# Optimization experiments

Hardware: AMD Instinct MI355X
Metric: run time of the kernel (lower is better)

The kernel has to match this reference:

```python
import jax, jax.numpy as jnp
import numpy as np

N = 50000      # nodes
E = 1600000    # edges (avg degree 32)
IN, H, OUT, ED = 16, 128, 64, 16


def setup_inputs() -> dict:
    key = jax.random.key(0)
    ks = jax.random.split(key, 24)

    def w(k, shape):
        return jax.random.normal(k, shape, jnp.float32) / np.float32(np.sqrt(shape[0]))

    inp = {
        "x": jax.random.normal(ks[0], (N, IN), jnp.float32),
        "edge_attr": jax.random.normal(ks[1], (E, ED), jnp.float32),
        "edge_src": jax.random.randint(ks[2], (E,), 0, N, jnp.int32),
        "edge_dst": jax.random.randint(ks[3], (E,), 0, N, jnp.int32),
    }
    dims = [(IN, H, H), (H, H, H), (H, H, OUT)]
    i = 4
    for l, (din, dh, dout) in enumerate(dims):
        inp[f"we{l}"] = w(ks[i], (ED, din)); inp[f"be{l}"] = jnp.zeros((din,), jnp.float32)
        inp[f"w1{l}"] = w(ks[i + 1], (din, dh)); inp[f"b1{l}"] = jnp.zeros((dh,), jnp.float32)
        inp[f"w2{l}"] = w(ks[i + 2], (dh, dout)); inp[f"b2{l}"] = jnp.zeros((dout,), jnp.float32)
        i += 3
    inp["rw1"] = w(ks[i], (OUT, H)); inp["rb1"] = jnp.zeros((H,), jnp.float32)
    inp["rw2"] = w(ks[i + 1], (H, IN)); inp["rb2"] = jnp.zeros((IN,), jnp.float32)
    return inp


def reference(x, edge_attr, edge_src, edge_dst,
              we0, be0, w10, b10, w20, b20,
              we1, be1, w11, b11, w21, b21,
              we2, be2, w12, b12, w22, b22,
              rw1, rb1, rw2, rb2):
    layers = [(we0, be0, w10, b10, w20, b20),
              (we1, be1, w11, b11, w21, b21),
              (we2, be2, w12, b12, w22, b22)]
    n = x.shape[0]

    def phi(h):
        # GIN with edge features (GINE): h_i = MLP(h_i + sum_j relu(h_j + W_e e_ij))
        for idx, (we, be, w1, b1, w2, b2) in enumerate(layers):
            e = edge_attr @ we + be                                  # [E, d_in]
            msg = jax.nn.relu(h[edge_src] + e)                       # [E, d_in]
            agg = jax.ops.segment_sum(msg, edge_dst, num_segments=n)  # [N, d_in]
            h = jax.nn.relu((h + agg) @ w1 + b1) @ w2 + b2           # conv MLP
            if idx < len(layers) - 1:
                h = jax.nn.relu(h)
        return h

    out = phi(x) + phi(-x)                       # sign invariance, [N, OUT]
    out = jax.nn.relu(out @ rw1 + rb1) @ rw2 + rb2  # rho readout, [N, IN]
    return out
```

## Files before the change

kernel.cpp:

```cpp
#include <hip/hip_runtime.h>

constexpr int DHID = 128;

typedef __attribute__((ext_vector_type(8))) short bf16x8v;
typedef __attribute__((ext_vector_type(4))) float f32x4v;

__device__ __forceinline__ float b2f(unsigned short u) {
    union { unsigned int i; float f; } v;
    v.i = ((unsigned int)u) << 16;
    return v.f;
}
__device__ __forceinline__ unsigned short f2b(float f) {
    union { float f; unsigned int i; } v;
    v.f = f;
    unsigned int x = v.i;
    return (unsigned short)((x + 0x7fff + ((x >> 16) & 1)) >> 16);
}
__device__ __forceinline__ unsigned int pack2(float a, float b) {
    return (unsigned int)f2b(a) | ((unsigned int)f2b(b) << 16);
}
__device__ __forceinline__ float bres(float w) { return w - b2f(f2b(w)); }
__device__ __forceinline__ void dot2b(float& acc, unsigned int a, unsigned int b) {
    asm("v_dot2_f32_bf16 %0, %1, %2, %0" : "+v"(acc) : "v"(a), "v"(b));
}

__global__ __launch_bounds__(256)
void init_h0(const float* __restrict__ x, float* __restrict__ H0,
             unsigned short* __restrict__ H0B, int n) {
    int i = blockIdx.x * 256 + threadIdx.x;
    if (i < n * 16) {
        int r = i >> 4, c = i & 15;
        float v = x[i];
        H0[(size_t)(2 * r) * 16 + c] = v;
        H0[(size_t)(2 * r + 1) * 16 + c] = -v;
        H0B[(size_t)(2 * r) * 16 + c] = f2b(v);
        H0B[(size_t)(2 * r + 1) * 16 + c] = f2b(-v);
    }
}

__global__ __launch_bounds__(256)
void sum_signs(const float* __restrict__ H3, float* __restrict__ S, int n) {
    int i = blockIdx.x * 256 + threadIdx.x;
    if (i < n * 64) {
        int r = i >> 6;
        S[i] = H3[i + (size_t)r * 64] + H3[i + (size_t)r * 64 + 64];
    }
}

__global__ __launch_bounds__(256)
void csr_count(const int* __restrict__ DST, int* __restrict__ deg, int E_) {
    int e = blockIdx.x * 256 + threadIdx.x;
    if (e < E_) atomicAdd(&deg[DST[e]], 1);
}

__global__ __launch_bounds__(256)
void scan1(const int* __restrict__ deg, int* __restrict__ off,
           int* __restrict__ bsum, int n) {
    __shared__ int s[256];
    int tid = threadIdx.x;
    int i = blockIdx.x * 256 + tid;
    int v = (i < n) ? deg[i] : 0;
    s[tid] = v;
    __syncthreads();
    for (int d = 1; d < 256; d <<= 1) {
        int t = (tid >= d) ? s[tid - d] : 0;
        __syncthreads();
        if (tid >= d) s[tid] += t;
        __syncthreads();
    }
    if (i < n) off[i] = s[tid] - v;
    if (tid == 255) bsum[blockIdx.x] = s[255];
}

__global__ __launch_bounds__(256)
void scan2(int* __restrict__ bsum, int nb) {
    __shared__ int s[256];
    int tid = threadIdx.x;
    int v = (tid < nb) ? bsum[tid] : 0;
    s[tid] = v;
    __syncthreads();
    for (int d = 1; d < 256; d <<= 1) {
        int t = (tid >= d) ? s[tid - d] : 0;
        __syncthreads();
        if (tid >= d) s[tid] += t;
        __syncthreads();
    }
    if (tid < nb) bsum[tid] = s[tid] - v;
}

__global__ __launch_bounds__(256)
void scan3(int* __restrict__ off, int* __restrict__ pos,
           const int* __restrict__ bsum, const int* __restrict__ deg, int n) {
    int i = blockIdx.x * 256 + threadIdx.x;
    if (i < n) {
        int o = off[i] + bsum[blockIdx.x];
        off[i] = o;
        pos[i] = o;
        if (i == n - 1) off[n] = o + deg[i];
    }
}

__global__ __launch_bounds__(256)
void csr_fill(const int* __restrict__ SRC, const int* __restrict__ DST,
              const float* __restrict__ EA, int* __restrict__ pos,
              int* __restrict__ csrsrc, uint4* __restrict__ EABS, int E_) {
    int e = blockIdx.x * 256 + threadIdx.x;
    if (e < E_) {
        int d = DST[e];
        int j = atomicAdd(&pos[d], 1);
        csrsrc[j] = SRC[e];
        const float4* ea4 = (const float4*)(EA + (size_t)e * 16);
        float4 q0 = ea4[0], q1 = ea4[1], q2 = ea4[2], q3 = ea4[3];
        uint4 o0, o1;
        o0.x = pack2(q0.x, q0.y); o0.y = pack2(q0.z, q0.w);
        o0.z = pack2(q1.x, q1.y); o0.w = pack2(q1.z, q1.w);
        o1.x = pack2(q2.x, q2.y); o1.y = pack2(q2.z, q2.w);
        o1.z = pack2(q3.x, q3.y); o1.w = pack2(q3.z, q3.w);
        EABS[(size_t)2 * j] = o0;
        EABS[(size_t)2 * j + 1] = o1;
    }
}

__global__ __launch_bounds__(256)
void agg_gather128(const int* __restrict__ CSRS, const int* __restrict__ OFF,
                   const unsigned short* __restrict__ EABS,
                   const float* __restrict__ WE, const float* __restrict__ BE,
                   const unsigned short* __restrict__ HB,
                   float* __restrict__ AGG, int n) {
    const int tid = threadIdx.x;
    const int lane = tid & 63;
    const int node = blockIdx.x * 4 + (tid >> 6);
    if (node >= n) return;
    const int col = lane & 15;
    const int grp = lane >> 4;
    const int klo = (grp & 1) * 8;

    bf16x8v bfrag[8];
#pragma unroll
    for (int cb = 0; cb < 8; ++cb) {
        bf16x8v b;
#pragma unroll
        for (int i = 0; i < 8; ++i) {
            float w = WE[(klo + i) * 128 + cb * 16 + col];
            unsigned short hi = f2b(w);
            unsigned short lo = f2b(bres(w));
            b[i] = (short)(grp >= 2 ? lo : hi);
        }
        bfrag[cb] = b;
    }
    float bias[8];
#pragma unroll
    for (int cb = 0; cb < 8; ++cb) bias[cb] = BE[cb * 16 + col];

    float asum0[8], asum1[8];
#pragma unroll
    for (int cb = 0; cb < 8; ++cb) { asum0[cb] = 0.f; asum1[cb] = 0.f; }

    const int j0 = OFF[node], j1 = OFF[node + 1];
    const char* ebase = (const char*)EABS;

    for (int base = j0; base < j1; base += 16) {
        const int rem = j1 - base;
        uint4 a4 = *(const uint4*)(ebase + ((size_t)(base + col) << 5) +
                                   ((grp & 1) << 4));
        bf16x8v afrag = __builtin_bit_cast(bf16x8v, a4);
        f32x4v ev[8];
#pragma unroll
        for (int cb = 0; cb < 8; ++cb) {
            f32x4v c = {bias[cb], bias[cb], bias[cb], bias[cb]};
            ev[cb] = __builtin_amdgcn_mfma_f32_16x16x32_bf16(afrag, bfrag[cb], c,
                                                             0, 0, 0);
        }
        float vmask[4];
        const unsigned short* hp[4];
#pragma unroll
        for (int r = 0; r < 4; ++r) {
            int t = grp * 4 + r;
            bool valid = t < rem;
            vmask[r] = valid ? 1.f : 0.f;
            int ji = valid ? (base + t) : j0;
            int src = CSRS[ji];
            hp[r] = HB + (size_t)(2 * src) * 128;
        }
#pragma unroll
        for (int cb = 0; cb < 8; ++cb) {
            float p0 = 0.f, p1 = 0.f;
#pragma unroll
            for (int r = 0; r < 4; ++r) {
                float e = ev[cb][r];
                float h0 = b2f(hp[r][cb * 16 + col]);
                float h1 = b2f(hp[r][128 + cb * 16 + col]);
                p0 += fmaxf(h0 + e, 0.f) * vmask[r];
                p1 += fmaxf(h1 + e, 0.f) * vmask[r];
            }
            p0 += __shfl_xor(p0, 16);
            p0 += __shfl_xor(p0, 32);
            p1 += __shfl_xor(p1, 16);
            p1 += __shfl_xor(p1, 32);
            asum0[cb] += p0;
            asum1[cb] += p1;
        }
    }
    float* arow = AGG + (size_t)(2 * node) * 128;
#pragma unroll
    for (int cb = 0; cb < 8; ++cb) {
        if (grp == (cb & 3)) {
            arow[cb * 16 + col] = asum0[cb];
            arow[128 + cb * 16 + col] = asum1[cb];
        }
    }
}

__global__ __launch_bounds__(256)
void agg_gather16(const int* __restrict__ CSRS, const int* __restrict__ OFF,
                  const uint4* __restrict__ EABS, const float* __restrict__ WE,
                  const float* __restrict__ BE,
                  const unsigned short* __restrict__ HB,
                  float* __restrict__ AGG, int n) {
    const int l = threadIdx.x & 31;
    const int node = blockIdx.x * 8 + (threadIdx.x >> 5);
    if (node >= n) return;
    const int s = l >> 4;
    const int c = l & 15;
    unsigned int wh[8], wl[8];
#pragma unroll
    for (int t = 0; t < 8; ++t) {
        float a0 = WE[(2 * t) * 16 + c], a1 = WE[(2 * t + 1) * 16 + c];
        wh[t] = pack2(a0, a1);
        wl[t] = pack2(bres(a0), bres(a1));
    }
    const float bev = BE[c];
    float acc = 0.f;
    const int j0 = OFF[node], j1 = OFF[node + 1];
#pragma unroll 4
    for (int j = j0; j < j1; ++j) {
        int src = CSRS[j];
        uint4 p = EABS[(size_t)2 * j], q = EABS[(size_t)2 * j + 1];
        float ec = bev;
        dot2b(ec, p.x, wh[0]); dot2b(ec, p.y, wh[1]);
        dot2b(ec, p.z, wh[2]); dot2b(ec, p.w, wh[3]);
        dot2b(ec, q.x, wh[4]); dot2b(ec, q.y, wh[5]);
        dot2b(ec, q.z, wh[6]); dot2b(ec, q.w, wh[7]);
        dot2b(ec, p.x, wl[0]); dot2b(ec, p.y, wl[1]);
        dot2b(ec, p.z, wl[2]); dot2b(ec, p.w, wl[3]);
        dot2b(ec, q.x, wl[4]); dot2b(ec, q.y, wl[5]);
        dot2b(ec, q.z, wl[6]); dot2b(ec, q.w, wl[7]);
        float hv = b2f(HB[(size_t)(2 * src + s) * 16 + c]);
        acc += fmaxf(hv + ec, 0.f);
    }
    AGG[(size_t)(2 * node + s) * 16 + c] = acc;
}

template <int DIN, int DOUT, bool RELU_OUT, bool HAS_AGG, bool WRITE_B>
__global__ __launch_bounds__(256)
void node_mlp(const float* __restrict__ X, const float* __restrict__ AGG,
              const float* __restrict__ W1, const float* __restrict__ B1,
              const float* __restrict__ W2, const float* __restrict__ B2,
              float* __restrict__ OUT, unsigned short* __restrict__ OUTB,
              int rows) {
    __shared__ float sX[32 * DIN];
    __shared__ float sH[32 * DHID];
    const int tid = threadIdx.x;

    for (int row0 = blockIdx.x * 32; row0 < rows; row0 += gridDim.x * 32) {
        __syncthreads();
        constexpr int DIN4 = DIN / 4;
        for (int i = tid; i < 32 * DIN4; i += 256) {
            int r = i / DIN4, k4 = i % DIN4;
            int gr = row0 + r;
            float4 v = make_float4(0.f, 0.f, 0.f, 0.f);
            if (gr < rows) {
                v = ((const float4*)X)[(size_t)gr * DIN4 + k4];
                if (HAS_AGG) {
                    float4 a = ((const float4*)AGG)[(size_t)gr * DIN4 + k4];
                    v.x += a.x; v.y += a.y; v.z += a.z; v.w += a.w;
                }
            }
            ((float4*)sX)[i] = v;
        }
        __syncthreads();
        {
            const int c = tid & 63;
            const int r0 = tid >> 6;
            float acc[8][2];
            const float b1a = B1[c], b1b = B1[c + 64];
#pragma unroll
            for (int j = 0; j < 8; ++j) {
                acc[j][0] = b1a;
                acc[j][1] = b1b;
            }
#pragma unroll 2
            for (int k4 = 0; k4 < DIN / 4; ++k4) {
                const int k = 4 * k4;
                float wa[4], wb[4];
#pragma unroll
                for (int kk = 0; kk < 4; ++kk) {
                    wa[kk] = W1[(k + kk) * DHID + c];
                    wb[kk] = W1[(k + kk) * DHID + c + 64];
                }
#pragma unroll
                for (int j = 0; j < 8; ++j) {
                    float4 xv = ((const float4*)sX)[((r0 + 4 * j) * DIN + k) >> 2];
                    acc[j][0] += xv.x * wa[0]; acc[j][1] += xv.x * wb[0];
                    acc[j][0] += xv.y * wa[1]; acc[j][1] += xv.y * wb[1];
                    acc[j][0] += xv.z * wa[2]; acc[j][1] += xv.z * wb[2];
                    acc[j][0] += xv.w * wa[3]; acc[j][1] += xv.w * wb[3];
                }
            }
#pragma unroll
            for (int j = 0; j < 8; ++j) {
                int r = r0 + 4 * j;
                sH[r * DHID + c] = fmaxf(acc[j][0], 0.f);
                sH[r * DHID + c + 64] = fmaxf(acc[j][1], 0.f);
            }
        }
        __syncthreads();
        {
            constexpr int HALF = DOUT / 2;
            constexpr int RP = 256 / HALF;
            constexpr int ITER = 32 / RP;
            const int c = tid % HALF;
            const int r0 = tid / HALF;
            float acc[ITER][2];
            const float bz0 = B2[c], bz1 = B2[c + HALF];
#pragma unroll
            for (int j = 0; j < ITER; ++j) {
                acc[j][0] = bz0;
                acc[j][1] = bz1;
            }
#pragma unroll 2
            for (int k4 = 0; k4 < DHID / 4; ++k4) {
                const int k = 4 * k4;
                float wa[4], wb[4];
#pragma unroll
                for (int kk = 0; kk < 4; ++kk) {
                    wa[kk] = W2[(k + kk) * DOUT + c];
                    wb[kk] = W2[(k + kk) * DOUT + c + HALF];
                }
#pragma unroll
                for (int j = 0; j < ITER; ++j) {
                    float4 hv = ((const float4*)sH)[((r0 + RP * j) * DHID + k) >> 2];
                    acc[j][0] += hv.x * wa[0]; acc[j][1] += hv.x * wb[0];
                    acc[j][0] += hv.y * wa[1]; acc[j][1] += hv.y * wb[1];
                    acc[j][0] += hv.z * wa[2]; acc[j][1] += hv.z * wb[2];
                    acc[j][0] += hv.w * wa[3]; acc[j][1] += hv.w * wb[3];
                }
            }
#pragma unroll
            for (int j = 0; j < ITER; ++j) {
                int gr = row0 + r0 + RP * j;
                if (gr < rows) {
                    float o0 = acc[j][0], o1 = acc[j][1];
                    if (RELU_OUT) {
                        o0 = fmaxf(o0, 0.f);
                        o1 = fmaxf(o1, 0.f);
                    }
                    OUT[(size_t)gr * DOUT + c] = o0;
                    OUT[(size_t)gr * DOUT + c + HALF] = o1;
                    if (WRITE_B) {
                        OUTB[(size_t)gr * DOUT + c] = f2b(o0);
                        OUTB[(size_t)gr * DOUT + c + HALF] = f2b(o1);
                    }
                }
            }
        }
    }
}

extern "C" void kernel_launch(void* const* d_in, const int* in_sizes, int n_in,
                              void* d_out, int out_size, void* d_ws, size_t ws_size,
                              hipStream_t stream) {
    const float* x = (const float*)d_in[0];
    const float* ea = (const float*)d_in[1];
    const int* esrc = (const int*)d_in[2];
    const int* edst = (const int*)d_in[3];
    const float* we0 = (const float*)d_in[4];
    const float* be0 = (const float*)d_in[5];
    const float* w10 = (const float*)d_in[6];
    const float* b10 = (const float*)d_in[7];
    const float* w20 = (const float*)d_in[8];
    const float* b20 = (const float*)d_in[9];
    const float* we1 = (const float*)d_in[10];
    const float* be1 = (const float*)d_in[11];
    const float* w11 = (const float*)d_in[12];
    const float* b11 = (const float*)d_in[13];
    const float* w21 = (const float*)d_in[14];
    const float* b21 = (const float*)d_in[15];
    const float* we2 = (const float*)d_in[16];
    const float* be2 = (const float*)d_in[17];
    const float* w12 = (const float*)d_in[18];
    const float* b12 = (const float*)d_in[19];
    const float* w22 = (const float*)d_in[20];
    const float* b22 = (const float*)d_in[21];
    const float* rw1 = (const float*)d_in[22];
    const float* rb1 = (const float*)d_in[23];
    const float* rw2 = (const float*)d_in[24];
    const float* rb2 = (const float*)d_in[25];

    const int N = in_sizes[0] / 16;
    const int E = in_sizes[2];
    const int M = 2 * N;

    float* HA = (float*)d_ws;
    float* HB = HA + (size_t)M * 128;
    float* AG = HB + (size_t)M * 128;
    unsigned short* Hb = (unsigned short*)(AG + (size_t)M * 128);
    unsigned short* EABS = Hb + (size_t)M * 128;
    int* deg = (int*)(EABS + (size_t)E * 16);
    int* off = deg + N;
    int* pos = off + N + 1;
    int* bsum = pos + N;
    int* csrsrc = bsum + 256;

    const int ntiles = (M + 31) / 32;
    const int eblocks = (E + 255) / 256;
    const int nblocks = (N + 255) / 256;

    hipMemsetAsync(deg, 0, (size_t)N * sizeof(int), stream);
    csr_count<<<eblocks, 256, 0, stream>>>(edst, deg, E);
    scan1<<<nblocks, 256, 0, stream>>>(deg, off, bsum, N);
    scan2<<<1, 256, 0, stream>>>(bsum, nblocks);
    scan3<<<nblocks, 256, 0, stream>>>(off, pos, bsum, deg, N);
    csr_fill<<<eblocks, 256, 0, stream>>>(esrc, edst, ea, pos, csrsrc,
                                          (uint4*)EABS, E);

    init_h0<<<(N * 16 + 255) / 256, 256, 0, stream>>>(x, HA, Hb, N);

    agg_gather16<<<(N + 7) / 8, 256, 0, stream>>>(csrsrc, off, (const uint4*)EABS,
                                                  we0, be0, Hb, AG, N);
    node_mlp<16, 128, true, true, true><<<ntiles, 256, 0, stream>>>(
        HA, AG, w10, b10, w20, b20, HB, Hb, M);

    agg_gather128<<<(N + 3) / 4, 256, 0, stream>>>(csrsrc, off, EABS,
                                                   we1, be1, Hb, AG, N);
    node_mlp<128, 128, true, true, true><<<ntiles, 256, 0, stream>>>(
        HB, AG, w11, b11, w21, b21, HA, Hb, M);

    agg_gather128<<<(N + 3) / 4, 256, 0, stream>>>(csrsrc, off, EABS,
                                                   we2, be2, Hb, AG, N);
    node_mlp<128, 64, false, true, false><<<ntiles, 256, 0, stream>>>(
        HA, AG, w12, b12, w22, b22, HB, nullptr, M);

    sum_signs<<<(N * 64 + 255) / 256, 256, 0, stream>>>(HB, AG, N);
    node_mlp<64, 16, false, false, false><<<(N + 31) / 32, 256, 0, stream>>>(
        AG, nullptr, rw1, rb1, rw2, rb2, (float*)d_out, nullptr, N);
}
```

Baseline: 1.006 ms.

## Replace scalar node MLP with split-bf16 MFMA matrix-core kernel

Rewrites the per-node two-layer MLP to use 16x16x32 bf16 MFMA instructions instead of scalar FP32 FMAs. Inputs, weights and hidden activations are split into high and low bf16 parts (lanes split between hi and residual terms) so that two MFMAs per K-chunk keep close to FP32 accuracy. Weights are loaded into register fragments once per block and the hidden layer is staged through LDS as bf16 hi/lo. The tile grows to 64 rows per block; the cost is register pressure from preloaded fragments and a small loss of precision.

```diff
diff --git a/kernel.cpp b/kernel.cpp
--- a/kernel.cpp
+++ b/kernel.cpp
@@ -253,114 +253,158 @@
 
 template <int DIN, int DOUT, bool RELU_OUT, bool HAS_AGG, bool WRITE_B>
 __global__ __launch_bounds__(256)
-void node_mlp(const float* __restrict__ X, const float* __restrict__ AGG,
-              const float* __restrict__ W1, const float* __restrict__ B1,
-              const float* __restrict__ W2, const float* __restrict__ B2,
-              float* __restrict__ OUT, unsigned short* __restrict__ OUTB,
-              int rows) {
-    __shared__ float sX[32 * DIN];
-    __shared__ float sH[32 * DHID];
+void node_mlp_mfma(const float* __restrict__ X, const float* __restrict__ AGG,
+                   const float* __restrict__ W1, const float* __restrict__ B1,
+                   const float* __restrict__ W2, const float* __restrict__ B2,
+                   float* __restrict__ OUT, unsigned short* __restrict__ OUTB,
+                   int rows) {
+    constexpr int KC1 = DIN / 16;
+    constexpr int NB2 = DOUT / 16;
+    constexpr int CB2W = (NB2 >= 4) ? NB2 / 4 : 1;
+    constexpr int SHS = 136;
+    __shared__ unsigned short sHhi[64 * SHS];
+    __shared__ unsigned short sHlo[64 * SHS];
     const int tid = threadIdx.x;
-
-    for (int row0 = blockIdx.x * 32; row0 < rows; row0 += gridDim.x * 32) {
-        __syncthreads();
-        constexpr int DIN4 = DIN / 4;
-        for (int i = tid; i < 32 * DIN4; i += 256) {
-            int r = i / DIN4, k4 = i % DIN4;
-            int gr = row0 + r;
-            float4 v = make_float4(0.f, 0.f, 0.f, 0.f);
-            if (gr < rows) {
-                v = ((const float4*)X)[(size_t)gr * DIN4 + k4];
+    const int w = tid >> 6;
+    const int lane = tid & 63;
+    const int col = lane & 15;
+    const int grp = lane >> 4;
+    const int khalf = (grp & 1) * 8;
+    const bool hi_lane = grp < 2;
+    const int row0 = blockIdx.x * 64;
+
+    bf16x8v b1f[2][KC1];
+    float bias1[2];
+#pragma unroll
+    for (int cb = 0; cb < 2; ++cb) {
+        const int cbg = 2 * w + cb;
+#pragma unroll
+        for (int kc = 0; kc < KC1; ++kc) {
+            bf16x8v b;
+#pragma unroll
+            for (int i = 0; i < 8; ++i) {
+                float wv = W1[(size_t)(kc * 16 + khalf + i) * DHID + cbg * 16 + col];
+                b[i] = (short)(hi_lane ? f2b(wv) : f2b(bres(wv)));
+            }
+            b1f[cb][kc] = b;
+        }
+        bias1[cb] = B1[cbg * 16 + col];
+    }
+
+#pragma unroll
+    for (int rg = 0; rg < 4; ++rg) {
+        bf16x8v a1[KC1], a2[KC1];
+        const int row = row0 + rg * 16 + col;
+        const bool rok = row < rows;
+#pragma unroll
+        for (int kc = 0; kc < KC1; ++kc) {
+            float xv[8];
+            if (rok) {
+                const float4* xp =
+                    (const float4*)(X + (size_t)row * DIN + kc * 16 + khalf);
+                float4 u0 = xp[0], u1 = xp[1];
                 if (HAS_AGG) {
-                    float4 a = ((const float4*)AGG)[(size_t)gr * DIN4 + k4];
-                    v.x += a.x; v.y += a.y; v.z += a.z; v.w += a.w;
+                    const float4* ap =
+                        (const float4*)(AGG + (size_t)row * DIN + kc * 16 + khalf);
+                    float4 g0 = ap[0], g1 = ap[1];
+                    u0.x += g0.x; u0.y += g0.y; u0.z += g0.z; u0.w += g0.w;
+                    u1.x += g1.x; u1.y += g1.y; u1.z += g1.z; u1.w += g1.w;
                 }
-            }
-            ((float4*)sX)[i] = v;
-        }
-        __syncthreads();
-        {
-            const int c = tid & 63;
-            const int r0 = tid >> 6;
-            float acc[8][2];
-            const float b1a = B1[c], b1b = B1[c + 64];
-#pragma unroll
-            for (int j = 0; j < 8; ++j) {
-                acc[j][0] = b1a;
-                acc[j][1] = b1b;
-            }
-#pragma unroll 2
-            for (int k4 = 0; k4 < DIN / 4; ++k4) {
-                const int k = 4 * k4;
-                float wa[4], wb[4];
-#pragma unroll
-                for (int kk = 0; kk < 4; ++kk) {
-                    wa[kk] = W1[(k + kk) * DHID + c];
-                    wb[kk] = W1[(k + kk) * DHID + c + 64];
-                }
-#pragma unroll
-                for (int j = 0; j < 8; ++j) {
-                    float4 xv = ((const float4*)sX)[((r0 + 4 * j) * DIN + k) >> 2];
-                    acc[j][0] += xv.x * wa[0]; acc[j][1] += xv.x * wb[0];
-                    acc[j][0] += xv.y * wa[1]; acc[j][1] += xv.y * wb[1];
-                    acc[j][0] += xv.z * wa[2]; acc[j][1] += xv.z * wb[2];
-                    acc[j][0] += xv.w * wa[3]; acc[j][1] += xv.w * wb[3];
-                }
-            }
-#pragma unroll
-            for (int j = 0; j < 8; ++j) {
-                int r = r0 + 4 * j;
-                sH[r * DHID + c] = fmaxf(acc[j][0], 0.f);
-                sH[r * DHID + c + 64] = fmaxf(acc[j][1], 0.f);
-            }
-        }
-        __syncthreads();
-        {
-            constexpr int HALF = DOUT / 2;
-            constexpr int RP = 256 / HALF;
-            constexpr int ITER = 32 / RP;
-            const int c = tid % HALF;
-            const int r0 = tid / HALF;
-            float acc[ITER][2];
-            const float bz0 = B2[c], bz1 = B2[c + HALF];
-#pragma unroll
-            for (int j = 0; j < ITER; ++j) {
-                acc[j][0] = bz0;
-                acc[j][1] = bz1;
-            }
-#pragma unroll 2
-            for (int k4 = 0; k4 < DHID / 4; ++k4) {
-                const int k = 4 * k4;
-                float wa[4], wb[4];
-#pragma unroll
-                for (int kk = 0; kk < 4; ++kk) {
-                    wa[kk] = W2[(k + kk) * DOUT + c];
-                    wb[kk] = W2[(k + kk) * DOUT + c + HALF];
-                }
-#pragma unroll
-                for (int j = 0; j < ITER; ++j) {
-                    float4 hv = ((const float4*)sH)[((r0 + RP * j) * DHID + k) >> 2];
-                    acc[j][0] += hv.x * wa[0]; acc[j][1] += hv.x * wb[0];
-                    acc[j][0] += hv.y * wa[1]; acc[j][1] += hv.y * wb[1];
-                    acc[j][0] += hv.z * wa[2]; acc[j][1] += hv.z * wb[2];
-                    acc[j][0] += hv.w * wa[3]; acc[j][1] += hv.w * wb[3];
-                }
-            }
-#pragma unroll
-            for (int j = 0; j < ITER; ++j) {
-                int gr = row0 + r0 + RP * j;
+                xv[0] = u0.x; xv[1] = u0.y; xv[2] = u0.z; xv[3] = u0.w;
+                xv[4] = u1.x; xv[5] = u1.y; xv[6] = u1.z; xv[7] = u1.w;
+            } else {
+#pragma unroll
+                for (int i = 0; i < 8; ++i) xv[i] = 0.f;
+            }
+            bf16x8v h, l;
+#pragma unroll
+            for (int i = 0; i < 8; ++i) {
+                unsigned short hv = f2b(xv[i]);
+                h[i] = (short)hv;
+                float r = xv[i] - b2f(hv);
+                l[i] = (short)(hi_lane ? f2b(r) : (unsigned short)0);
+            }
+            a1[kc] = h;
+            a2[kc] = l;
+        }
+#pragma unroll
+        for (int cb = 0; cb < 2; ++cb) {
+            const int cbg = 2 * w + cb;
+            f32x4v acc = {bias1[cb], bias1[cb], bias1[cb], bias1[cb]};
+#pragma unroll
+            for (int kc = 0; kc < KC1; ++kc) {
+                acc = __builtin_amdgcn_mfma_f32_16x16x32_bf16(a1[kc], b1f[cb][kc],
+                                                              acc, 0, 0, 0);
+                acc = __builtin_amdgcn_mfma_f32_16x16x32_bf16(a2[kc], b1f[cb][kc],
+                                                              acc, 0, 0, 0);
+            }
+#pragma unroll
+            for (int r = 0; r < 4; ++r) {
+                float v = fmaxf(acc[r], 0.f);
+                unsigned short hv = f2b(v);
+                float res = v - b2f(hv);
+                const int row_l = rg * 16 + grp * 4 + r;
+                sHhi[row_l * SHS + cbg * 16 + col] = hv;
+                sHlo[row_l * SHS + cbg * 16 + col] = f2b(res);
+            }
+        }
+    }
+
+    bf16x8v b2fr[CB2W][8];
+    float bias2[CB2W];
+#pragma unroll
+    for (int cj = 0; cj < CB2W; ++cj) {
+        const int cb2g = (NB2 >= 4) ? (w * CB2W + cj) : 0;
+#pragma unroll
+        for (int kc = 0; kc < 8; ++kc) {
+            bf16x8v b;
+#pragma unroll
+            for (int i = 0; i < 8; ++i) {
+                float wv = W2[(size_t)(kc * 16 + khalf + i) * DOUT + cb2g * 16 + col];
+                b[i] = (short)(hi_lane ? f2b(wv) : f2b(bres(wv)));
+            }
+            b2fr[cj][kc] = b;
+        }
+        bias2[cj] = B2[cb2g * 16 + col];
+    }
+    __syncthreads();
+
+    const int rg_lo = (NB2 == 1) ? w : 0;
+    const int rg_hi = (NB2 == 1) ? w + 1 : 4;
+    for (int rg = rg_lo; rg < rg_hi; ++rg) {
+        bf16x8v a1[8], a2[8];
+#pragma unroll
+        for (int kc = 0; kc < 8; ++kc) {
+            const int addr = (rg * 16 + col) * SHS + kc * 16 + khalf;
+            a1[kc] = *(const bf16x8v*)&sHhi[addr];
+            if (hi_lane) {
+                a2[kc] = *(const bf16x8v*)&sHlo[addr];
+            } else {
+                bf16x8v z;
+#pragma unroll
+                for (int i = 0; i < 8; ++i) z[i] = 0;
+                a2[kc] = z;
+            }
+        }
+#pragma unroll
+        for (int cj = 0; cj < CB2W; ++cj) {
+            const int cb2g = (NB2 >= 4) ? (w * CB2W + cj) : 0;
+            f32x4v acc = {bias2[cj], bias2[cj], bias2[cj], bias2[cj]};
+#pragma unroll
+            for (int kc = 0; kc < 8; ++kc) {
+                acc = __builtin_amdgcn_mfma_f32_16x16x32_bf16(a1[kc], b2fr[cj][kc],
+                                                              acc, 0, 0, 0);
+                acc = __builtin_amdgcn_mfma_f32_16x16x32_bf16(a2[kc], b2fr[cj][kc],
+                                                              acc, 0, 0, 0);
+            }
+#pragma unroll
+            for (int r = 0; r < 4; ++r) {
+                const int gr = row0 + rg * 16 + grp * 4 + r;
                 if (gr < rows) {
-                    float o0 = acc[j][0], o1 = acc[j][1];
-                    if (RELU_OUT) {
-                        o0 = fmaxf(o0, 0.f);
-                        o1 = fmaxf(o1, 0.f);
-                    }
-                    OUT[(size_t)gr * DOUT + c] = o0;
-                    OUT[(size_t)gr * DOUT + c + HALF] = o1;
-                    if (WRITE_B) {
-                        OUTB[(size_t)gr * DOUT + c] = f2b(o0);
-                        OUTB[(size_t)gr * DOUT + c + HALF] = f2b(o1);
-                    }
+                    float o = acc[r];
+                    if (RELU_OUT) o = fmaxf(o, 0.f);
+                    OUT[(size_t)gr * DOUT + cb2g * 16 + col] = o;
+                    if (WRITE_B) OUTB[(size_t)gr * DOUT + cb2g * 16 + col] = f2b(o);
                 }
             }
         }
@@ -412,9 +456,9 @@
     int* bsum = pos + N;
     int* csrsrc = bsum + 256;
 
-    const int ntiles = (M + 31) / 32;
     const int eblocks = (E + 255) / 256;
     const int nblocks = (N + 255) / 256;
+    const int mt = (M + 63) / 64;
 
     hipMemsetAsync(deg, 0, (size_t)N * sizeof(int), stream);
     csr_count<<<eblocks, 256, 0, stream>>>(edst, deg, E);
@@ -428,20 +472,20 @@
 
     agg_gather16<<<(N + 7) / 8, 256, 0, stream>>>(csrsrc, off, (const uint4*)EABS,
                                                   we0, be0, Hb, AG, N);
-    node_mlp<16, 128, true, true, true><<<ntiles, 256, 0, stream>>>(
+    node_mlp_mfma<16, 128, true, true, true><<<mt, 256, 0, stream>>>(
         HA, AG, w10, b10, w20, b20, HB, Hb, M);
 
     agg_gather128<<<(N + 3) / 4, 256, 0, stream>>>(csrsrc, off, EABS,
                                                    we1, be1, Hb, AG, N);
-    node_mlp<128, 128, true, true, true><<<ntiles, 256, 0, stream>>>(
+    node_mlp_mfma<128, 128, true, true, true><<<mt, 256, 0, stream>>>(
         HB, AG, w11, b11, w21, b21, HA, Hb, M);
 
     agg_gather128<<<(N + 3) / 4, 256, 0, stream>>>(csrsrc, off, EABS,
                                                    we2, be2, Hb, AG, N);
-    node_mlp<128, 64, false, true, false><<<ntiles, 256, 0, stream>>>(
+    node_mlp_mfma<128, 64, false, true, false><<<mt, 256, 0, stream>>>(
         HA, AG, w12, b12, w22, b22, HB, nullptr, M);
 
     sum_signs<<<(N * 64 + 255) / 256, 256, 0, stream>>>(HB, AG, N);
-    node_mlp<64, 16, false, false, false><<<(N + 31) / 32, 256, 0, stream>>>(
+    node_mlp_mfma<64, 16, false, false, false><<<(N + 63) / 64, 256, 0, stream>>>(
         AG, nullptr, rw1, rb1, rw2, rb2, (float*)d_out, nullptr, N);
 }
```

After: 1.609 ms. 1.6x slower.

## Stage MFMA edge features in LDS and vectorize neighbor row gathers

Applied to the files above, without the earlier changes.

In the 128-wide aggregation kernel, the per-edge edge-feature projection from MFMA is now written to a per-wave shared-memory tile. Each lane then reads 8 contiguous bf16 values of a neighbor's hidden row with one 16-byte load, instead of scalar 2-byte loads spread across MFMA output lanes. Invalid edge slots are masked by storing a large negative value, so the relu yields zero. This removes the per-column cross-lane shuffle reductions and makes the final AGG stores float4-wide. The cost is extra LDS traffic and an LDS round trip per edge chunk, and it relies on in-wave ordering of LDS accesses with no explicit barrier.

```diff
diff --git a/kernel.cpp b/kernel.cpp
--- a/kernel.cpp
+++ b/kernel.cpp
@@ -127,10 +127,14 @@
                    const float* __restrict__ WE, const float* __restrict__ BE,
                    const unsigned short* __restrict__ HB,
                    float* __restrict__ AGG, int n) {
+    __shared__ float esm_all[4][16][132];
     const int tid = threadIdx.x;
+    const int wv = tid >> 6;
     const int lane = tid & 63;
-    const int node = blockIdx.x * 4 + (tid >> 6);
+    const int node = blockIdx.x * 4 + wv;
     if (node >= n) return;
+    float (*esm)[132] = esm_all[wv];
+
     const int col = lane & 15;
     const int grp = lane >> 4;
     const int klo = (grp & 1) * 8;
@@ -152,9 +156,14 @@
 #pragma unroll
     for (int cb = 0; cb < 8; ++cb) bias[cb] = BE[cb * 16 + col];
 
-    float asum0[8], asum1[8];
-#pragma unroll
-    for (int cb = 0; cb < 8; ++cb) { asum0[cb] = 0.f; asum1[cb] = 0.f; }
+    const int o = lane & 31;
+    const int s = o >> 4;
+    const int co = (o & 15) * 8;
+    const int ep = lane >> 5;
+
+    float acc[8];
+#pragma unroll
+    for (int i = 0; i < 8; ++i) acc[i] = 0.f;
 
     const int j0 = OFF[node], j1 = OFF[node + 1];
     const char* ebase = (const char*)EABS;
@@ -164,50 +173,43 @@
         uint4 a4 = *(const uint4*)(ebase + ((size_t)(base + col) << 5) +
                                    ((grp & 1) << 4));
         bf16x8v afrag = __builtin_bit_cast(bf16x8v, a4);
-        f32x4v ev[8];
 #pragma unroll
         for (int cb = 0; cb < 8; ++cb) {
             f32x4v c = {bias[cb], bias[cb], bias[cb], bias[cb]};
-            ev[cb] = __builtin_amdgcn_mfma_f32_16x16x32_bf16(afrag, bfrag[cb], c,
-                                                             0, 0, 0);
-        }
-        float vmask[4];
-        const unsigned short* hp[4];
-#pragma unroll
-        for (int r = 0; r < 4; ++r) {
-            int t = grp * 4 + r;
-            bool valid = t < rem;
-            vmask[r] = valid ? 1.f : 0.f;
-            int ji = valid ? (base + t) : j0;
-            int src = CSRS[ji];
-            hp[r] = HB + (size_t)(2 * src) * 128;
-        }
-#pragma unroll
-        for (int cb = 0; cb < 8; ++cb) {
-            float p0 = 0.f, p1 = 0.f;
+            f32x4v ev = __builtin_amdgcn_mfma_f32_16x16x32_bf16(afrag, bfrag[cb],
+                                                                c, 0, 0, 0);
 #pragma unroll
             for (int r = 0; r < 4; ++r) {
-                float e = ev[cb][r];
-                float h0 = b2f(hp[r][cb * 16 + col]);
-                float h1 = b2f(hp[r][128 + cb * 16 + col]);
-                p0 += fmaxf(h0 + e, 0.f) * vmask[r];
-                p1 += fmaxf(h1 + e, 0.f) * vmask[r];
-            }
-            p0 += __shfl_xor(p0, 16);
-            p0 += __shfl_xor(p0, 32);
-            p1 += __shfl_xor(p1, 16);
-            p1 += __shfl_xor(p1, 32);
-            asum0[cb] += p0;
-            asum1[cb] += p1;
-        }
-    }
-    float* arow = AGG + (size_t)(2 * node) * 128;
-#pragma unroll
-    for (int cb = 0; cb < 8; ++cb) {
-        if (grp == (cb & 3)) {
-            arow[cb * 16 + col] = asum0[cb];
-            arow[128 + cb * 16 + col] = asum1[cb];
-        }
+                const int slot = grp * 4 + r;
+                esm[slot][cb * 16 + col] = (slot < rem) ? ev[r] : -1e30f;
+            }
+        }
+#pragma unroll
+        for (int i = 0; i < 8; ++i) {
+            const int er = 2 * i + ep;
+            const int eidx = base + er;
+            const int src = CSRS[eidx < j1 ? eidx : (j1 - 1)];
+            uint4 hv = *(const uint4*)(HB + (((size_t)(2 * src + s)) << 7) + co);
+            const float4* ep4 = (const float4*)&esm[er][co];
+            float4 e0 = ep4[0], e1 = ep4[1];
+            acc[0] += fmaxf(b2f(hv.x & 0xffff) + e0.x, 0.f);
+            acc[1] += fmaxf(b2f(hv.x >> 16)    + e0.y, 0.f);
+            acc[2] += fmaxf(b2f(hv.y & 0xffff) + e0.z, 0.f);
+            acc[3] += fmaxf(b2f(hv.y >> 16)    + e0.w, 0.f);
+            acc[4] += fmaxf(b2f(hv.z & 0xffff) + e1.x, 0.f);
+            acc[5] += fmaxf(b2f(hv.z >> 16)    + e1.y, 0.f);
+            acc[6] += fmaxf(b2f(hv.w & 0xffff) + e1.z, 0.f);
+            acc[7] += fmaxf(b2f(hv.w >> 16)    + e1.w, 0.f);
+        }
+    }
+#pragma unroll
+    for (int i = 0; i < 8; ++i) acc[i] += __shfl_xor(acc[i], 32);
+    if (lane < 32) {
+        float* arow = AGG + (size_t)(2 * node + s) * 128 + co;
+        float4 v0 = make_float4(acc[0], acc[1], acc[2], acc[3]);
+        float4 v1 = make_float4(acc[4], acc[5], acc[6], acc[7]);
+        ((float4*)arow)[0] = v0;
+        ((float4*)arow)[1] = v1;
     }
 }
 
```

After: 955.0 us. 5.0% less time.
